# Kernel tuning notes

Hardware: AMD Instinct MI355X
Metric: run time of the kernel (lower is better)

Reference implementation:

```python
import jax, jax.numpy as jnp
import numpy as np

EMB = 1024
HEADS = 16
HEAD_DIM = EMB // HEADS
MASK_VAL = -10000.0


def setup_inputs() -> dict:
    key = jax.random.key(0)
    ks = jax.random.split(key, 5)
    B, S = 4, 2048
    x = jax.random.normal(ks[0], (B, S, EMB), dtype=jnp.float32)
    scale = 1.0 / np.sqrt(EMB)
    w_qkv = jax.random.normal(ks[1], (EMB, 3 * EMB), dtype=jnp.float32) * scale
    b_qkv = jnp.zeros((3 * EMB,), dtype=jnp.float32)
    w_fc = jax.random.normal(ks[2], (EMB, EMB), dtype=jnp.float32) * scale
    b_fc = jnp.zeros((EMB,), dtype=jnp.float32)
    return {"x": x, "w_qkv": w_qkv, "b_qkv": b_qkv, "w_fc": w_fc, "b_fc": b_fc}


def reference(x, w_qkv, b_qkv, w_fc, b_fc):
    B, S, _ = x.shape
    qkv = x @ w_qkv + b_qkv                      # (B, S, 3*EMB)
    q, k, v = jnp.split(qkv, 3, axis=-1)
    # split heads: (B, S, EMB) -> (B, H, S, Dh)
    def sh(t):
        return t.reshape(B, S, HEADS, HEAD_DIM).transpose(0, 2, 1, 3)
    q, k, v = sh(q), sh(k), sh(v)
    scores = jnp.einsum('bhqd,bhkd->bhqk', q, k) / np.sqrt(HEAD_DIM)
    causal = jnp.tril(jnp.ones((S, S), dtype=bool))[None, None]
    scores = jnp.where(causal, scores, jnp.float32(MASK_VAL))
    probs = jax.nn.softmax(scores, axis=-1)
    out = jnp.einsum('bhqk,bhkd->bhqd', probs, v)
    out = out.transpose(0, 2, 1, 3).reshape(B, S, EMB)  # merge heads
    return out @ w_fc + b_fc
```

## Files before the change

kernel.cpp:

```cpp
#include <hip/hip_runtime.h>
#include <hip/hip_bf16.h>
#include <cstdint>

#define BF16 __hip_bfloat16

typedef __attribute__((ext_vector_type(8))) short bhalf8;
typedef __attribute__((ext_vector_type(4))) float floatx4;

#define MFMA16(a, b, c) __builtin_amdgcn_mfma_f32_16x16x32_bf16((a), (b), (c), 0, 0, 0)

#define MASKV (-30000.0f)
#define QSCALE 0.18033688011112042f

__device__ __forceinline__ bhalf8 cvt8(const float* p) {
  const float4 f0 = *(const float4*)p;
  const float4 f1 = *(const float4*)(p + 4);
  union { bhalf8 v; ushort u[8]; } r;
  const float t[8] = {f0.x, f0.y, f0.z, f0.w, f1.x, f1.y, f1.z, f1.w};
#pragma unroll
  for (int i = 0; i < 8; ++i) {
    BF16 h = __float2bfloat16(t[i]);
    r.u[i] = *(const ushort*)&h;
  }
  return r.v;
}

__global__ void cvt_f32_bf16(const float* __restrict__ in, BF16* __restrict__ out) {
  const size_t i = ((size_t)blockIdx.x * 256 + threadIdx.x) * 8;
  *(bhalf8*)(out + i) = cvt8(in + i);
}

__global__ void transpose_cvt(const float* __restrict__ in, ushort* __restrict__ out,
                              int R, int C) {
  __shared__ ushort t[32][33];
  const int c0 = blockIdx.x * 32, r0 = blockIdx.y * 32;
  const int tx = threadIdx.x, ty = threadIdx.y;
#pragma unroll
  for (int j = 0; j < 32; j += 8) {
    BF16 h = __float2bfloat16(in[(size_t)(r0 + ty + j) * C + c0 + tx]);
    t[ty + j][tx] = *(const ushort*)&h;
  }
  __syncthreads();
#pragma unroll
  for (int j = 0; j < 32; j += 8)
    out[(size_t)(c0 + ty + j) * R + r0 + tx] = t[tx][ty + j];
}

template <int MODE>
__global__ __launch_bounds__(256, 2) void gemm_bt(
    const BF16* __restrict__ A, const BF16* __restrict__ Bt, const float* __restrict__ bias,
    void* __restrict__ C0v, BF16* __restrict__ C1, BF16* __restrict__ C2,
    int Md, int Nd, int Kd) {
  __shared__ __align__(16) BF16 As[128 * 64];
  __shared__ __align__(16) BF16 Bs[128 * 64];

  const int tid = threadIdx.x;
  const int w = tid >> 6, lane = tid & 63;
  const int lm = lane & 15, quad = lane >> 4;
  const int wm = (w >> 1) * 64, wn = (w & 1) * 64;

  const int lin = blockIdx.y * gridDim.x + blockIdx.x;
  const int per8 = (gridDim.x * gridDim.y) >> 3;
  const int swz = (lin & 7) * per8 + (lin >> 3);
  const int tile_m = (swz / gridDim.x) * 128, tile_n = (swz % gridDim.x) * 128;

  floatx4 acc[4][4];
#pragma unroll
  for (int i = 0; i < 4; ++i)
#pragma unroll
    for (int j = 0; j < 4; ++j) acc[i][j] = (floatx4){0.f, 0.f, 0.f, 0.f};

  int srow[4], sgs[4], sslot[4];
#pragma unroll
  for (int j = 0; j < 4; ++j) {
    const int slot = (j * 4 + w) * 64 + lane;
    sslot[j] = slot;
    srow[j] = slot >> 3;
    sgs[j] = ((slot & 7) - (slot >> 3)) & 7;
  }

  bhalf8 va[4], vb[4], nva[4], nvb[4];
#pragma unroll
  for (int j = 0; j < 4; ++j) {
    va[j] = *(const bhalf8*)(A + (size_t)(tile_m + srow[j]) * Kd + sgs[j] * 8);
    vb[j] = *(const bhalf8*)(Bt + (size_t)(tile_n + srow[j]) * Kd + sgs[j] * 8);
  }

  for (int k0 = 0; k0 < Kd; k0 += 64) {
    __syncthreads();
#pragma unroll
    for (int j = 0; j < 4; ++j) {
      *(bhalf8*)(As + sslot[j] * 8) = va[j];
      *(bhalf8*)(Bs + sslot[j] * 8) = vb[j];
    }
    __syncthreads();

    if (k0 + 64 < Kd) {
      const int k1 = k0 + 64;
#pragma unroll
      for (int j = 0; j < 4; ++j) {
        nva[j] = *(const bhalf8*)(A + (size_t)(tile_m + srow[j]) * Kd + k1 + sgs[j] * 8);
        nvb[j] = *(const bhalf8*)(Bt + (size_t)(tile_n + srow[j]) * Kd + k1 + sgs[j] * 8);
      }
    }

#pragma unroll
    for (int s = 0; s < 2; ++s) {
      bhalf8 af[4], bfr[4];
#pragma unroll
      for (int mt = 0; mt < 4; ++mt) {
        const int r = wm + mt * 16 + lm;
        const int g = ((s * 4 + quad) + r) & 7;
        af[mt] = *(const bhalf8*)(As + r * 64 + g * 8);
      }
#pragma unroll
      for (int nt = 0; nt < 4; ++nt) {
        const int r = wn + nt * 16 + lm;
        const int g = ((s * 4 + quad) + r) & 7;
        bfr[nt] = *(const bhalf8*)(Bs + r * 64 + g * 8);
      }
#pragma unroll
      for (int mt = 0; mt < 4; ++mt)
#pragma unroll
        for (int nt = 0; nt < 4; ++nt)
          acc[mt][nt] = MFMA16(af[mt], bfr[nt], acc[mt][nt]);
    }
#pragma unroll
    for (int j = 0; j < 4; ++j) { va[j] = nva[j]; vb[j] = nvb[j]; }
  }

#pragma unroll
  for (int nt = 0; nt < 4; ++nt) {
    const int n = tile_n + wn + nt * 16 + lm;
    const float bv = bias[n];
#pragma unroll
    for (int mt = 0; mt < 4; ++mt) {
      const int m0 = tile_m + wm + mt * 16 + quad * 4;
      floatx4 v = acc[mt][nt];
      if (MODE == 0) {
        float* C0f = (float*)C0v;
#pragma unroll
        for (int r = 0; r < 4; ++r)
          C0f[(size_t)(m0 + r) * Nd + n] = v[r] + bv;
      } else {
        const int which = n >> 10;
        const int h = (n >> 6) & 15;
        const int d = n & 63;
        if (which == 2) {
          const int b = m0 >> 11, s0 = m0 & 2047;
          union { ushort4 u4; ushort u[4]; } pk;
#pragma unroll
          for (int r = 0; r < 4; ++r) {
            BF16 hv = __float2bfloat16(v[r] + bv);
            pk.u[r] = *(const ushort*)&hv;
          }
          *(ushort4*)(C2 + ((size_t)((b * 16 + h) * 64 + d)) * 2048 + s0) = pk.u4;
        } else {
          BF16* dst = (which == 0) ? (BF16*)C0v : C1;
          const float sc = (which == 0) ? QSCALE : 1.0f;
#pragma unroll
          for (int r = 0; r < 4; ++r) {
            const int m = m0 + r, b = m >> 11, si = m & 2047;
            dst[((size_t)(b * 16 + h) * 2048 + si) * 64 + d] =
                __float2bfloat16((v[r] + bv) * sc);
          }
        }
      }
    }
  }
}

__global__ __launch_bounds__(256, 2) void flash_attn(
    const BF16* __restrict__ Q, const BF16* __restrict__ Kmat,
    const BF16* __restrict__ VT, BF16* __restrict__ O) {
  __shared__ __align__(16) BF16 Ps[4][4][16 * 64];

  const int tid = threadIdx.x;
  const int w = tid >> 6, lane = tid & 63;
  const int lm = lane & 15, quad = lane >> 4;

  const int bid = blockIdx.x;
  const int xcd = bid & 7;
  const int li = bid >> 3;
  const int bh = xcd * 8 + (li >> 3);
  const int x = li & 7;

  const int sel = (w + x) & 3;
  const int qt = (sel == 0) ? x : (sel == 1) ? (15 - x) : (sel == 2) ? (16 + x) : (31 - x);
  const int qb0 = qt * 64;
  const size_t bh_off = (size_t)bh * (2048 * 64);

  union { bhalf8 v; ushort u[8]; } onesu;
#pragma unroll
  for (int i = 0; i < 8; ++i) onesu.u[i] = 0x3F80;
  const bhalf8 ones8 = onesu.v;

  bhalf8 aq[4][2];
#pragma unroll
  for (int s2 = 0; s2 < 4; ++s2) {
    const BF16* qp = Q + bh_off + (size_t)(qb0 + s2 * 16 + lm) * 64 + quad * 8;
    aq[s2][0] = *(const bhalf8*)qp;
    aq[s2][1] = *(const bhalf8*)(qp + 32);
  }

  floatx4 oacc[4][4];
  float m_i[4], l_i[4];
#pragma unroll
  for (int s2 = 0; s2 < 4; ++s2) {
    m_i[s2] = MASKV;
    l_i[s2] = 0.f;
#pragma unroll
    for (int i = 0; i < 4; ++i) oacc[s2][i] = (floatx4){0.f, 0.f, 0.f, 0.f};
  }

  for (int kt = 0; kt <= qt; ++kt) {
    const int k0 = kt * 64;

    bhalf8 ak[4][2], av[4][2];
#pragma unroll
    for (int nt = 0; nt < 4; ++nt) {
      const BF16* kp = Kmat + bh_off + (size_t)(k0 + nt * 16 + lm) * 64 + quad * 8;
      ak[nt][0] = *(const bhalf8*)kp;
      ak[nt][1] = *(const bhalf8*)(kp + 32);
      const BF16* vp = VT + bh_off + (size_t)(nt * 16 + lm) * 2048 + k0 + quad * 8;
      av[nt][0] = *(const bhalf8*)vp;
      av[nt][1] = *(const bhalf8*)(vp + 32);
    }

#pragma unroll
    for (int s2 = 0; s2 < 4; ++s2) {
      const int qb = qb0 + s2 * 16;

      floatx4 st[4];
      __builtin_amdgcn_s_setprio(1);
#pragma unroll
      for (int nt = 0; nt < 4; ++nt) {
        floatx4 z = (floatx4){0.f, 0.f, 0.f, 0.f};
        z = MFMA16(ak[nt][0], aq[s2][0], z);
        z = MFMA16(ak[nt][1], aq[s2][1], z);
        st[nt] = z;
      }
      __builtin_amdgcn_s_setprio(0);

      if (k0 + 63 > qb) {
#pragma unroll
        for (int nt = 0; nt < 4; ++nt)
#pragma unroll
          for (int r = 0; r < 4; ++r)
            if ((k0 + nt * 16 + quad * 4 + r) > (qb + lm)) st[nt][r] = MASKV;
      }

      float a0 = fmaxf(st[0][0], st[0][1]), a1 = fmaxf(st[0][2], st[0][3]);
      float a2 = fmaxf(st[1][0], st[1][1]), a3 = fmaxf(st[1][2], st[1][3]);
      float a4 = fmaxf(st[2][0], st[2][1]), a5 = fmaxf(st[2][2], st[2][3]);
      float a6 = fmaxf(st[3][0], st[3][1]), a7 = fmaxf(st[3][2], st[3][3]);
      float b0 = fmaxf(a0, a1), b1 = fmaxf(a2, a3);
      float b2 = fmaxf(a4, a5), b3 = fmaxf(a6, a7);
      float mx = fmaxf(fmaxf(b0, b1), fmaxf(b2, b3));
      mx = fmaxf(mx, __shfl_xor(mx, 16, 64));
      mx = fmaxf(mx, __shfl_xor(mx, 32, 64));

      if (!__all(mx <= m_i[s2] + 8.0f)) {
        const float mnew = fmaxf(m_i[s2], mx);
        const float alpha = __builtin_amdgcn_exp2f(m_i[s2] - mnew);
        m_i[s2] = mnew;
        l_i[s2] *= alpha;
#pragma unroll
        for (int dn = 0; dn < 4; ++dn) oacc[s2][dn] *= alpha;
      }

#pragma unroll
      for (int nt = 0; nt < 4; ++nt)
#pragma unroll
        for (int r = 0; r < 4; ++r)
          st[nt][r] = __builtin_amdgcn_exp2f(st[nt][r] - m_i[s2]);

      {
        BF16* pws = Ps[w][s2];
#pragma unroll
        for (int nt = 0; nt < 4; ++nt) {
          union { ushort4 u4; ushort u[4]; } pk;
#pragma unroll
          for (int r = 0; r < 4; ++r) {
            BF16 h = __float2bfloat16(st[nt][r]);
            pk.u[r] = *(const ushort*)&h;
          }
          const int g = ((nt * 2 + (quad >> 1)) + lm) & 7;
          *(ushort4*)(pws + lm * 64 + g * 8 + (quad & 1) * 4) = pk.u4;
        }
      }

      if (s2 > 0) {
        const int sp = s2 - 1;
        const BF16* pwp = Ps[w][sp];
        const bhalf8 ap0 = *(const bhalf8*)(pwp + lm * 64 + ((quad + lm) & 7) * 8);
        const bhalf8 ap1 = *(const bhalf8*)(pwp + lm * 64 + ((4 + quad + lm) & 7) * 8);
        __builtin_amdgcn_s_setprio(1);
        floatx4 zl = (floatx4){0.f, 0.f, 0.f, 0.f};
        zl = MFMA16(ones8, ap0, zl);
        zl = MFMA16(ones8, ap1, zl);
#pragma unroll
        for (int dn = 0; dn < 4; ++dn) {
          oacc[sp][dn] = MFMA16(av[dn][0], ap0, oacc[sp][dn]);
          oacc[sp][dn] = MFMA16(av[dn][1], ap1, oacc[sp][dn]);
        }
        __builtin_amdgcn_s_setprio(0);
        l_i[sp] += zl[0];
      }
    }

    {
      const BF16* pwp = Ps[w][3];
      const bhalf8 ap0 = *(const bhalf8*)(pwp + lm * 64 + ((quad + lm) & 7) * 8);
      const bhalf8 ap1 = *(const bhalf8*)(pwp + lm * 64 + ((4 + quad + lm) & 7) * 8);
      __builtin_amdgcn_s_setprio(1);
      floatx4 zl = (floatx4){0.f, 0.f, 0.f, 0.f};
      zl = MFMA16(ones8, ap0, zl);
      zl = MFMA16(ones8, ap1, zl);
#pragma unroll
      for (int dn = 0; dn < 4; ++dn) {
        oacc[3][dn] = MFMA16(av[dn][0], ap0, oacc[3][dn]);
        oacc[3][dn] = MFMA16(av[dn][1], ap1, oacc[3][dn]);
      }
      __builtin_amdgcn_s_setprio(0);
      l_i[3] += zl[0];
    }
  }

  const int b = bh >> 4, h = bh & 15;
#pragma unroll
  for (int s2 = 0; s2 < 4; ++s2) {
    const float inv_l = 1.0f / l_i[s2];
    const size_t orow = (size_t)(b * 2048 + qb0 + s2 * 16 + lm) * 1024 + h * 64;
#pragma unroll
    for (int dn = 0; dn < 4; ++dn) {
      union { ushort4 u4; ushort u[4]; } pk;
#pragma unroll
      for (int r = 0; r < 4; ++r) {
        BF16 h2 = __float2bfloat16(oacc[s2][dn][r] * inv_l);
        pk.u[r] = *(const ushort*)&h2;
      }
      *(ushort4*)(O + orow + dn * 16 + quad * 4) = pk.u4;
    }
  }
}

extern "C" void kernel_launch(void* const* d_in, const int* in_sizes, int n_in,
                              void* d_out, int out_size, void* d_ws, size_t ws_size,
                              hipStream_t stream) {
  const float* x = (const float*)d_in[0];
  const float* w_qkv = (const float*)d_in[1];
  const float* b_qkv = (const float*)d_in[2];
  const float* w_fc = (const float*)d_in[3];
  const float* b_fc = (const float*)d_in[4];
  float* out = (float*)d_out;

  BF16* ws = (BF16*)d_ws;
  BF16* wTqkv = ws;
  BF16* wTfc = wTqkv + 3072 * 1024;
  BF16* xb = wTfc + 1024 * 1024;
  BF16* Qb = xb + 8388608;
  BF16* Kb = Qb + 8388608;
  BF16* VTb = Kb + 8388608;
  BF16* Ob = VTb + 8388608;

  cvt_f32_bf16<<<4096, 256, 0, stream>>>(x, xb);
  transpose_cvt<<<dim3(96, 32), dim3(32, 8), 0, stream>>>(w_qkv, (ushort*)wTqkv, 1024, 3072);
  transpose_cvt<<<dim3(32, 32), dim3(32, 8), 0, stream>>>(w_fc, (ushort*)wTfc, 1024, 1024);

  gemm_bt<1><<<dim3(24, 64), 256, 0, stream>>>(
      xb, wTqkv, b_qkv, (void*)Qb, Kb, VTb, 8192, 3072, 1024);
  flash_attn<<<dim3(512), 256, 0, stream>>>(Qb, Kb, VTb, Ob);
  gemm_bt<0><<<dim3(8, 64), 256, 0, stream>>>(
      Ob, wTfc, b_fc, (void*)out, nullptr, nullptr, 8192, 1024, 1024);
}
```

Before: 283.1 us.

## Add 256x256-tile QKV GEMM with direct global-to-LDS triple-buffered loads

Replaces the QKV projection GEMM with a new kernel that uses 256x256 output tiles, 512 threads, and a three-stage LDS ring filled by global_load_lds instructions with a swizzled layout and an XCD-aware block remap. Larger tiles raise arithmetic intensity and cut redundant global reads, and the async direct-to-LDS loads overlap memory traffic with MFMA work. In exchange it needs many accumulator registers (128 floats per thread) and only 384 blocks, which may reduce occupancy and leave CUs unevenly loaded on the tail.

```diff
diff --git a/kernel.cpp b/kernel.cpp
--- a/kernel.cpp
+++ b/kernel.cpp
@@ -11,6 +11,11 @@
 
 #define MASKV (-30000.0f)
 #define QSCALE 0.18033688011112042f
+
+#define GLOAD_LDS16(g, l)                                   \
+  __builtin_amdgcn_global_load_lds(                         \
+      (const __attribute__((address_space(1))) void*)(g),   \
+      (__attribute__((address_space(3))) void*)(l), 16, 0, 0)
 
 __device__ __forceinline__ bhalf8 cvt8(const float* p) {
   const float4 f0 = *(const float4*)p;
@@ -170,6 +175,130 @@
   }
 }
 
+__global__ __launch_bounds__(512, 2) void gemm_qkv256(
+    const BF16* __restrict__ A, const BF16* __restrict__ Bt, const float* __restrict__ bias,
+    BF16* __restrict__ Qo, BF16* __restrict__ Ko, BF16* __restrict__ Vo, int Kd) {
+  __shared__ __align__(16) BF16 As[3][256 * 32];
+  __shared__ __align__(16) BF16 Bs[3][256 * 32];
+
+  const int tid = threadIdx.x;
+  const int w = tid >> 6, lane = tid & 63;
+  const int lm = lane & 15, quad = lane >> 4;
+  const int wm = w >> 2, wn = w & 3;
+
+  const int lin = blockIdx.y * gridDim.x + blockIdx.x;
+  const int per8 = (gridDim.x * gridDim.y) >> 3;
+  const int swz = (lin & 7) * per8 + (lin >> 3);
+  const int tile_m = (swz / gridDim.x) * 256, tile_n = (swz % gridDim.x) * 256;
+
+  const int NT = Kd >> 5;
+
+  int srow[2], skg[2];
+#pragma unroll
+  for (int j = 0; j < 2; ++j) {
+    const int slot = j * 512 + tid;
+    srow[j] = slot >> 2;
+    skg[j] = ((slot & 3) - ((slot >> 3) & 3)) & 3;
+  }
+  const int dst0 = w * 64;
+
+  floatx4 acc[8][4];
+#pragma unroll
+  for (int mt = 0; mt < 8; ++mt)
+#pragma unroll
+    for (int nt = 0; nt < 4; ++nt) acc[mt][nt] = (floatx4){0.f, 0.f, 0.f, 0.f};
+
+#pragma unroll
+  for (int t = 0; t < 2; ++t) {
+#pragma unroll
+    for (int j = 0; j < 2; ++j) {
+      GLOAD_LDS16(A + (size_t)(tile_m + srow[j]) * Kd + t * 32 + skg[j] * 8,
+                  As[t] + (j * 512 + dst0) * 8);
+      GLOAD_LDS16(Bt + (size_t)(tile_n + srow[j]) * Kd + t * 32 + skg[j] * 8,
+                  Bs[t] + (j * 512 + dst0) * 8);
+    }
+  }
+
+  int bc = 0, bs = 2;
+  for (int t = 0; t < NT; ++t) {
+    __builtin_amdgcn_sched_barrier(0);
+    __builtin_amdgcn_s_barrier();
+    if (t + 1 < NT) {
+      asm volatile("s_waitcnt vmcnt(4)" ::: "memory");
+    } else {
+      asm volatile("s_waitcnt vmcnt(0)" ::: "memory");
+    }
+
+    if (t + 2 < NT) {
+#pragma unroll
+      for (int j = 0; j < 2; ++j) {
+        GLOAD_LDS16(A + (size_t)(tile_m + srow[j]) * Kd + (t + 2) * 32 + skg[j] * 8,
+                    As[bs] + (j * 512 + dst0) * 8);
+        GLOAD_LDS16(Bt + (size_t)(tile_n + srow[j]) * Kd + (t + 2) * 32 + skg[j] * 8,
+                    Bs[bs] + (j * 512 + dst0) * 8);
+      }
+    }
+
+    bhalf8 af[8], bfv[4];
+#pragma unroll
+    for (int mt = 0; mt < 8; ++mt) {
+      const int r = wm * 128 + mt * 16 + lm;
+      const int g = (quad + ((r >> 1) & 3)) & 3;
+      af[mt] = *(const bhalf8*)(As[bc] + r * 32 + g * 8);
+    }
+#pragma unroll
+    for (int nt = 0; nt < 4; ++nt) {
+      const int r = wn * 64 + nt * 16 + lm;
+      const int g = (quad + ((r >> 1) & 3)) & 3;
+      bfv[nt] = *(const bhalf8*)(Bs[bc] + r * 32 + g * 8);
+    }
+
+    __builtin_amdgcn_s_setprio(1);
+#pragma unroll
+    for (int mt = 0; mt < 8; ++mt)
+#pragma unroll
+      for (int nt = 0; nt < 4; ++nt)
+        acc[mt][nt] = MFMA16(af[mt], bfv[nt], acc[mt][nt]);
+    __builtin_amdgcn_s_setprio(0);
+
+    bc = (bc == 2) ? 0 : bc + 1;
+    bs = (bs == 2) ? 0 : bs + 1;
+  }
+
+#pragma unroll
+  for (int nt = 0; nt < 4; ++nt) {
+    const int n = tile_n + wn * 64 + nt * 16 + lm;
+    const float bv = bias[n];
+    const int which = n >> 10;
+    const int h = (n >> 6) & 15;
+    const int d = n & 63;
+#pragma unroll
+    for (int mt = 0; mt < 8; ++mt) {
+      const int m0 = tile_m + wm * 128 + mt * 16 + quad * 4;
+      floatx4 v = acc[mt][nt];
+      if (which == 2) {
+        const int b = m0 >> 11, s0 = m0 & 2047;
+        union { ushort4 u4; ushort u[4]; } pk;
+#pragma unroll
+        for (int r = 0; r < 4; ++r) {
+          BF16 hv = __float2bfloat16(v[r] + bv);
+          pk.u[r] = *(const ushort*)&hv;
+        }
+        *(ushort4*)(Vo + ((size_t)((b * 16 + h) * 64 + d)) * 2048 + s0) = pk.u4;
+      } else {
+        BF16* dst = (which == 0) ? Qo : Ko;
+        const float sc = (which == 0) ? QSCALE : 1.0f;
+#pragma unroll
+        for (int r = 0; r < 4; ++r) {
+          const int m = m0 + r, b = m >> 11, si = m & 2047;
+          dst[((size_t)(b * 16 + h) * 2048 + si) * 64 + d] =
+              __float2bfloat16((v[r] + bv) * sc);
+        }
+      }
+    }
+  }
+}
+
 __global__ __launch_bounds__(256, 2) void flash_attn(
     const BF16* __restrict__ Q, const BF16* __restrict__ Kmat,
     const BF16* __restrict__ VT, BF16* __restrict__ O) {
@@ -368,8 +497,7 @@
   transpose_cvt<<<dim3(96, 32), dim3(32, 8), 0, stream>>>(w_qkv, (ushort*)wTqkv, 1024, 3072);
   transpose_cvt<<<dim3(32, 32), dim3(32, 8), 0, stream>>>(w_fc, (ushort*)wTfc, 1024, 1024);
 
-  gemm_bt<1><<<dim3(24, 64), 256, 0, stream>>>(
-      xb, wTqkv, b_qkv, (void*)Qb, Kb, VTb, 8192, 3072, 1024);
+  gemm_qkv256<<<dim3(12, 32), 512, 0, stream>>>(xb, wTqkv, b_qkv, Qb, Kb, VTb, 1024);
   flash_attn<<<dim3(512), 256, 0, stream>>>(Qb, Kb, VTb, Ob);
   gemm_bt<0><<<dim3(8, 64), 256, 0, stream>>>(
       Ob, wTfc, b_fc, (void*)out, nullptr, nullptr, 8192, 1024, 1024);
```

After: 303.4 us. +7.2%, slower.
